# Kernel optimization log

Hardware: AMD Instinct MI355X
Metric: run time of the kernel (lower is better)

The kernel has to match this reference:

```python
import jax, jax.numpy as jnp
import numpy as np

E, D, H, T = 8, 1024, 2048, 2048  # num_expert, d_model, d_hidden, tokens

def setup_inputs() -> dict:
    key = jax.random.key(0)
    ks = jax.random.split(key, 7)
    return {
        "moe_inp": jax.random.normal(ks[0], (T, D), jnp.float32),
        "Wg": jax.random.normal(ks[1], (D, E), jnp.float32) * 0.02,
        "bg": jnp.zeros((E,), jnp.float32),
        "W1": jax.random.normal(ks[2], (E, D, H), jnp.float32) * 0.02,
        "b1": jnp.zeros((E, H), jnp.float32),
        "W2": jax.random.normal(ks[3], (E, H, D), jnp.float32) * 0.02,
        "b2": jnp.zeros((E, D), jnp.float32),
        "top_k": 2,
    }

def reference(moe_inp, Wg, bg, W1, b1, W2, b2, top_k):
    # NaiveGate: linear gate, top-k select, softmax over the selected logits
    logits = moe_inp @ Wg + bg                      # [T, E]
    top_vals, top_idx = jax.lax.top_k(logits, top_k)  # [T, k]
    gate_score = jax.nn.softmax(top_vals, axis=-1)    # [T, k]

    # Exact (no capacity drop) MoE: scan over experts, mask-combine.
    # Equivalent math to scatter -> per-expert FFN -> gather -> bmm(gate_score, ...).
    def body(acc, xs):
        e, w1, bb1, w2, bb2 = xs
        h = jax.nn.gelu(moe_inp @ w1 + bb1)          # [T, H]
        y = h @ w2 + bb2                             # [T, D]
        w = jnp.sum(jnp.where(top_idx == e, gate_score, 0.0), axis=-1)  # [T]
        return acc + w[:, None] * y, None

    init = jnp.zeros_like(moe_inp)
    xs = (jnp.arange(E), W1, b1, W2, b2)
    moe_outp, _ = jax.lax.scan(body, init, xs)
    return moe_outp, top_idx
```

## Files before the change

kernel.cpp:

```cpp
#include <hip/hip_runtime.h>
#include <stdint.h>

#define T_TOK 2048
#define D_DIM 1024
#define H_DIM 2048
#define N_EXP 8
#define MAXS  4608

#define WS_CNT    0
#define WS_BTOK   256
#define WS_BW     (WS_BTOK + N_EXP*2048*4)
#define WS_XG     (WS_BW + N_EXP*2048*4)
#define WS_HBUF   (WS_XG + (size_t)MAXS*1024*2)
#define WS_W1T    (WS_HBUF + (size_t)MAXS*2048*2)
#define WS_W2T    (WS_W1T + (size_t)N_EXP*1024*2048*2)

typedef __bf16 bf16x8 __attribute__((ext_vector_type(8)));
typedef float  f32x4  __attribute__((ext_vector_type(4)));

#define AS1 __attribute__((address_space(1)))
#define AS3 __attribute__((address_space(3)))

__device__ __forceinline__ unsigned short f2bf(float f) {
  unsigned int u = __float_as_uint(f);
  u += 0x7fffu + ((u >> 16) & 1u);
  return (unsigned short)(u >> 16);
}

__device__ __forceinline__ float gelu_tanh(float x) {
  const float u = 0.7978845608028654f * (x + 0.044715f * x * x * x);
  const float t = __expf(-2.0f * fabsf(u));
  const float th = (1.0f - t) * __builtin_amdgcn_rcpf(1.0f + t);
  return 0.5f * x * (1.0f + copysignf(th, u));
}


__device__ __forceinline__ void transpose_body(const float* __restrict__ in,
                                               unsigned short* __restrict__ out,
                                               int Rout, int Cin, int tx, int ty,
                                               void* smem_) {
  char* lds = (char*)smem_;
  const int c0 = tx * 64, r0 = ty * 64;
  const int tid = threadIdx.x;
  const int w = tid >> 6, l = tid & 63;
  const int lr = l >> 4;
  const int lc4 = (l & 15) * 4;
#pragma unroll
  for (int p = 0; p < 4; ++p) {
    const int rr = p * 16 + w * 4 + lr;
    const int c = lc4 ^ ((rr & 7) << 2);
    const float* src = in + (size_t)(r0 + rr) * Cin + (c0 + c);
    __builtin_amdgcn_global_load_lds((const AS1 void*)src,
                                     (AS3 void*)(lds + (size_t)rr * 256 + lc4 * 4),
                                     16, 0, 0);
  }
  __syncthreads();
  unsigned u[2][4];
#pragma unroll
  for (int p = 0; p < 2; ++p) {
    const int idx = p * 256 + tid;
    const int oc = idx >> 3, seg = idx & 7;
#pragma unroll
    for (int j = 0; j < 4; ++j) {
      const int ra = seg * 8 + 2 * j, rb = ra + 1;
      const float va = *(const float*)(lds + ra * 256 + ((oc ^ ((ra & 7) << 2)) * 4));
      const float vb = *(const float*)(lds + rb * 256 + ((oc ^ ((rb & 7) << 2)) * 4));
      u[p][j] = (unsigned)f2bf(va) | ((unsigned)f2bf(vb) << 16);
    }
  }
#pragma unroll
  for (int p = 0; p < 2; ++p) {
    const int idx = p * 256 + tid;
    const int oc = idx >> 3, seg = idx & 7;
    *(uint4*)(out + (size_t)(c0 + oc) * Rout + r0 + seg * 8) =
        make_uint4(u[p][0], u[p][1], u[p][2], u[p][3]);
  }
}

__device__ __forceinline__ void gate_body(int t, const float* __restrict__ x,
                                          const float* __restrict__ Wg,
                                          const float* __restrict__ bg,
                                          float* __restrict__ out_idx,
                                          int* __restrict__ cnt, int* __restrict__ btok,
                                          float* __restrict__ bw) {
  const int lane = threadIdx.x & 63;
  float p[8];
#pragma unroll
  for (int i = 0; i < 8; ++i) p[i] = 0.f;
  const float* xr = x + (size_t)t * D_DIM;
  for (int i = lane; i < D_DIM; i += 64) {
    const float xv = xr[i];
    const float4 wa = ((const float4*)(Wg + i * 8))[0];
    const float4 wb = ((const float4*)(Wg + i * 8))[1];
    p[0] += xv * wa.x; p[1] += xv * wa.y; p[2] += xv * wa.z; p[3] += xv * wa.w;
    p[4] += xv * wb.x; p[5] += xv * wb.y; p[6] += xv * wb.z; p[7] += xv * wb.w;
  }
#pragma unroll
  for (int off = 32; off > 0; off >>= 1) {
#pragma unroll
    for (int i = 0; i < 8; ++i) p[i] += __shfl_xor(p[i], off);
  }
  if (lane == 0) {
#pragma unroll
    for (int i = 0; i < 8; ++i) p[i] += bg[i];
    int i0 = 0; float v0 = p[0];
#pragma unroll
    for (int i = 1; i < 8; ++i) if (p[i] > v0) { v0 = p[i]; i0 = i; }
    int i1 = -1; float v1 = -3.4e38f;
#pragma unroll
    for (int i = 0; i < 8; ++i) if (i != i0 && p[i] > v1) { v1 = p[i]; i1 = i; }
    const float ex = expf(v1 - v0);
    const float inv = 1.f / (1.f + ex);
    out_idx[t * 2 + 0] = (float)i0;
    out_idx[t * 2 + 1] = (float)i1;
    int s0 = atomicAdd(&cnt[i0], 1);
    btok[i0 * 2048 + s0] = t; bw[i0 * 2048 + s0] = inv;
    int s1 = atomicAdd(&cnt[i1], 1);
    btok[i1 * 2048 + s1] = t; bw[i1 * 2048 + s1] = ex * inv;
  }
}

__device__ __forceinline__ void expert_seg(const int* __restrict__ cnt, int e,
                                           int& base, int& ce, int& pcnt, int& total) {
  int off = 0; base = 0; ce = 0; pcnt = 0;
#pragma unroll
  for (int i = 0; i < N_EXP; ++i) {
    const int c = cnt[i];
    const int p = (c + 63) & ~63;
    if (i == e) { base = off; ce = c; pcnt = p; }
    off += p;
  }
  total = off;
}

template <int MODE>
__device__ __forceinline__ void gemm_body(
    int lin, const float* __restrict__ X, const unsigned short* __restrict__ A,
    const unsigned short* __restrict__ B,
    const float* __restrict__ bias, const int* __restrict__ cnt,
    const int* __restrict__ btok, const float* __restrict__ bw,
    unsigned short* __restrict__ Hout, float* __restrict__ out, void* smem_) {
  constexpr int K   = (MODE == 0) ? D_DIM : H_DIM;
  constexpr int SK  = (MODE == 0) ? 1 : 2;
  constexpr int KS  = K / SK;
  constexpr int NIT = KS / 32;

  const int glo = lin & 7;
  const int mt  = (lin >> 3) & 31;
  const int g   = ((lin >> 8) << 3) | glo;
  int nt, e, ksl;
  if (MODE == 0) { nt = g & 15; e = g >> 4; ksl = 0; }
  else           { nt = g & 7;  e = (g >> 3) & 7; ksl = g >> 6; }

  int base, ce, pcnt, total;
  expert_seg(cnt, e, base, ce, pcnt, total);
  if (mt * 64 >= pcnt) return;
  const int row0 = base + mt * 64;
  const int n0 = nt * 128;

  unsigned short (*As)[64 * 32] = (unsigned short (*)[64 * 32])smem_;
  unsigned short (*Bs)[128 * 32] = (unsigned short (*)[128 * 32])((char*)smem_ + 8192);

  const int tid = threadIdx.x;
  const int lane = tid & 63;
  const int wv = tid >> 6;
  const int wm = wv >> 1;
  const int wn = wv & 1;

  const unsigned short* Bb = B + (size_t)e * ((size_t)H_DIM * D_DIM) + (size_t)n0 * K + ksl * KS;

  f32x4 acc[2][4];
#pragma unroll
  for (int i = 0; i < 2; ++i)
#pragma unroll
    for (int j = 0; j < 4; ++j) acc[i][j] = (f32x4)(0.0f);

  const int subr = lane >> 2;
  const int ksf = (lane & 3) * 8;
  const int fr = lane & 15;
  const int kq = (lane >> 4) * 8;

  const unsigned short* Ab = nullptr;
  const float* a_src = nullptr;
  bool a_real = false;
  if constexpr (MODE == 0) {
    const int al = mt * 64 + wv * 16 + subr;
    a_real = (al < ce);
    const int tok = a_real ? btok[e * 2048 + al] : 0;
    a_src = X + (size_t)tok * D_DIM + ksf;
  } else {
    Ab = A + (size_t)row0 * K + ksl * KS;
  }

  float4 pa0, pa1;
  auto stageA_load = [&](int kt) {
    if constexpr (MODE == 0) {
      if (a_real) {
        pa0 = *(const float4*)(a_src + kt * 32);
        pa1 = *(const float4*)(a_src + kt * 32 + 4);
      } else {
        pa0 = make_float4(0.f, 0.f, 0.f, 0.f);
        pa1 = make_float4(0.f, 0.f, 0.f, 0.f);
      }
    }
  };
  auto stageA_write = [&](int b) {
    if constexpr (MODE == 0) {
      uint4 u;
      u.x = (unsigned)f2bf(pa0.x) | ((unsigned)f2bf(pa0.y) << 16);
      u.y = (unsigned)f2bf(pa0.z) | ((unsigned)f2bf(pa0.w) << 16);
      u.z = (unsigned)f2bf(pa1.x) | ((unsigned)f2bf(pa1.y) << 16);
      u.w = (unsigned)f2bf(pa1.z) | ((unsigned)f2bf(pa1.w) << 16);
      *(uint4*)(As[b] + (wv * 16 + subr) * 32 + ksf) = u;
    }
  };
  auto stage = [&](int kt, int b) {
    const int k0 = kt * 32;
    if constexpr (MODE == 1) {
      const int r = wv * 16 + subr;
      const unsigned short* ga = Ab + (size_t)r * K + (k0 + ksf);
      __builtin_amdgcn_global_load_lds(
          (const AS1 void*)ga,
          (AS3 void*)(As[b] + wv * 16 * 32), 16, 0, 0);
    }
#pragma unroll
    for (int it = 0; it < 2; ++it) {
      const int ci = wv + it * 4;
      const int r = ci * 16 + subr;
      const unsigned short* gb = Bb + (size_t)r * K + (k0 + ksf);
      __builtin_amdgcn_global_load_lds(
          (const AS1 void*)gb,
          (AS3 void*)(Bs[b] + ci * 16 * 32), 16, 0, 0);
    }
  };

  stageA_load(0);
  stage(0, 0);
  stageA_write(0);
  for (int i = 0; i < NIT; ++i) {
    const int b = i & 1;
    __syncthreads();
    if (i + 1 < NIT) { stageA_load(i + 1); stage(i + 1, b ^ 1); }
    bf16x8 av[2], bv[4];
#pragma unroll
    for (int mi = 0; mi < 2; ++mi)
      av[mi] = *(const bf16x8*)(As[b] + (wm * 32 + mi * 16 + fr) * 32 + kq);
#pragma unroll
    for (int ni = 0; ni < 4; ++ni)
      bv[ni] = *(const bf16x8*)(Bs[b] + (wn * 64 + ni * 16 + fr) * 32 + kq);
#pragma unroll
    for (int mi = 0; mi < 2; ++mi)
#pragma unroll
      for (int ni = 0; ni < 4; ++ni)
        acc[mi][ni] = __builtin_amdgcn_mfma_f32_16x16x32_bf16(av[mi], bv[ni], acc[mi][ni], 0, 0, 0);
    if (i + 1 < NIT) stageA_write(b ^ 1);
  }

  if (MODE == 0) {
    const float* bb = bias + (size_t)e * H_DIM + n0;
#pragma unroll
    for (int mi = 0; mi < 2; ++mi) {
      const int rb = wm * 32 + mi * 16 + (lane >> 4) * 4;
#pragma unroll
      for (int r = 0; r < 4; ++r) {
        unsigned short* hp = Hout + (size_t)(row0 + rb + r) * H_DIM + n0;
#pragma unroll
        for (int ni = 0; ni < 4; ++ni) {
          const int col = wn * 64 + ni * 16 + fr;
          hp[col] = f2bf(gelu_tanh(acc[mi][ni][r] + bb[col]));
        }
      }
    }
  } else {
    const float* bb = bias + (size_t)e * D_DIM + n0;
#pragma unroll
    for (int mi = 0; mi < 2; ++mi) {
      const int rb = wm * 32 + mi * 16 + (lane >> 4) * 4;
#pragma unroll
      for (int r = 0; r < 4; ++r) {
        const int local = mt * 64 + rb + r;
        if (local < ce) {
          const int tok = btok[e * 2048 + local];
          const float w = bw[e * 2048 + local];
          float* op = out + (size_t)tok * D_DIM + n0;
#pragma unroll
          for (int ni = 0; ni < 4; ++ni) {
            const int col = wn * 64 + ni * 16 + fr;
            const float bias_once = (ksl == 0) ? bb[col] : 0.f;
            atomicAdd(op + col, w * (acc[mi][ni][r] + bias_once));
          }
        }
      }
    }
  }
}


__global__ void __launch_bounds__(256) prep_kernel(
    const float* __restrict__ x, const float* __restrict__ Wg,
    const float* __restrict__ bg, const float* __restrict__ W1,
    float* __restrict__ out, int* __restrict__ cnt, int* __restrict__ btok,
    float* __restrict__ bw, unsigned short* __restrict__ W1t) {
  __shared__ __align__(16) char smem[16384];
  const int bid = blockIdx.x;
  if (bid < 2048) {
    ((float4*)out)[bid * 256 + threadIdx.x] = make_float4(0.f, 0.f, 0.f, 0.f);
  } else if (bid < 2560) {
    gate_body((bid - 2048) * 4 + (threadIdx.x >> 6), x, Wg, bg,
              out + (size_t)T_TOK * D_DIM, cnt, btok, bw);
  } else {
    const int lin = bid - 2560;
    const int e = lin >> 9, l9 = lin & 511;
    transpose_body(W1 + (size_t)e * (D_DIM * H_DIM), W1t + (size_t)e * (D_DIM * H_DIM),
                   D_DIM, H_DIM, l9 & 31, l9 >> 5, smem);
  }
}

__global__ void __launch_bounds__(256) gemm0_w2t(
    const float* __restrict__ x, const unsigned short* __restrict__ W1t,
    const float* __restrict__ b1, const int* __restrict__ cnt,
    const int* __restrict__ btok, const float* __restrict__ bw,
    unsigned short* __restrict__ Hbuf, const float* __restrict__ W2,
    unsigned short* __restrict__ W2t) {
  __shared__ __align__(16) char smem[24576];
  if (blockIdx.x < 4096) {
    gemm_body<0>(blockIdx.x, x, nullptr, W1t, b1, cnt, btok, bw, Hbuf, nullptr, smem);
  } else {
    const int lin = blockIdx.x - 4096;
    const int e = lin >> 9, l9 = lin & 511;
    transpose_body(W2 + (size_t)e * (D_DIM * H_DIM), W2t + (size_t)e * (D_DIM * H_DIM),
                   H_DIM, D_DIM, l9 & 15, l9 >> 4, smem);
  }
}

__global__ void __launch_bounds__(256) moe_gemm1(
    const unsigned short* __restrict__ Hbuf, const unsigned short* __restrict__ W2t,
    const float* __restrict__ b2, const int* __restrict__ cnt,
    const int* __restrict__ btok, const float* __restrict__ bw,
    float* __restrict__ out) {
  __shared__ __align__(16) char smem[24576];
  gemm_body<1>(blockIdx.x, nullptr, Hbuf, W2t, b2, cnt, btok, bw, nullptr, out, smem);
}

extern "C" void kernel_launch(void* const* d_in, const int* in_sizes, int n_in,
                              void* d_out, int out_size, void* d_ws, size_t ws_size,
                              hipStream_t stream) {
  const float* moe_inp = (const float*)d_in[0];
  const float* Wg = (const float*)d_in[1];
  const float* bg = (const float*)d_in[2];
  const float* W1 = (const float*)d_in[3];
  const float* b1 = (const float*)d_in[4];
  const float* W2 = (const float*)d_in[5];
  const float* b2 = (const float*)d_in[6];
  float* out = (float*)d_out;

  char* ws = (char*)d_ws;
  int* cnt  = (int*)(ws + WS_CNT);
  int* btok = (int*)(ws + WS_BTOK);
  float* bw = (float*)(ws + WS_BW);
  unsigned short* Hbuf = (unsigned short*)(ws + WS_HBUF);
  unsigned short* W1t  = (unsigned short*)(ws + WS_W1T);
  unsigned short* W2t  = (unsigned short*)(ws + WS_W2T);

  hipMemsetAsync(cnt, 0, 256, stream);
  prep_kernel<<<dim3(6656), dim3(256), 0, stream>>>(moe_inp, Wg, bg, W1,
                                                    out, cnt, btok, bw, W1t);
  gemm0_w2t<<<dim3(8192), dim3(256), 0, stream>>>(moe_inp, W1t, b1, cnt, btok, bw,
                                                  Hbuf, W2, W2t);
  moe_gemm1<<<dim3(4096), dim3(256), 0, stream>>>(Hbuf, W2t, b2, cnt, btok, bw, out);
}
```

Measured before the change: 319.7 us.

## Merge three MoE kernels into one cooperative persistent kernel with grid syncs

Replaces the memset plus three kernel launches with a single cooperative persistent kernel. It walks the zero-init, gate/W1-transpose, GEMM0/W2-transpose and GEMM1 phases in grid-stride loops, with grid.sync between phases. The weight transpose also changes from direct global-to-LDS async loads with XOR swizzle to plain float4 loads into a padded LDS tile. The aim is to remove launch gaps and tail effects between stages, at the cost of grid-wide barriers, a grid sized by the occupancy query, and possibly slower transpose loads.

```diff
diff --git a/kernel.cpp b/kernel.cpp
--- a/kernel.cpp
+++ b/kernel.cpp
@@ -1,5 +1,8 @@
 #include <hip/hip_runtime.h>
+#include <hip/hip_cooperative_groups.h>
 #include <stdint.h>
+
+namespace cg = cooperative_groups;
 
 #define T_TOK 2048
 #define D_DIM 1024
@@ -39,41 +42,28 @@
                                                unsigned short* __restrict__ out,
                                                int Rout, int Cin, int tx, int ty,
                                                void* smem_) {
-  char* lds = (char*)smem_;
+  float (*tile)[68] = (float (*)[68])smem_;
   const int c0 = tx * 64, r0 = ty * 64;
   const int tid = threadIdx.x;
-  const int w = tid >> 6, l = tid & 63;
-  const int lr = l >> 4;
-  const int lc4 = (l & 15) * 4;
 #pragma unroll
   for (int p = 0; p < 4; ++p) {
-    const int rr = p * 16 + w * 4 + lr;
-    const int c = lc4 ^ ((rr & 7) << 2);
-    const float* src = in + (size_t)(r0 + rr) * Cin + (c0 + c);
-    __builtin_amdgcn_global_load_lds((const AS1 void*)src,
-                                     (AS3 void*)(lds + (size_t)rr * 256 + lc4 * 4),
-                                     16, 0, 0);
+    const int idx = p * 256 + tid;
+    const int r = idx >> 4, c4 = idx & 15;
+    *(float4*)&tile[r][c4 * 4] = *(const float4*)(in + (size_t)(r0 + r) * Cin + c0 + c4 * 4);
   }
   __syncthreads();
-  unsigned u[2][4];
 #pragma unroll
   for (int p = 0; p < 2; ++p) {
     const int idx = p * 256 + tid;
     const int oc = idx >> 3, seg = idx & 7;
+    unsigned u[4];
 #pragma unroll
     for (int j = 0; j < 4; ++j) {
-      const int ra = seg * 8 + 2 * j, rb = ra + 1;
-      const float va = *(const float*)(lds + ra * 256 + ((oc ^ ((ra & 7) << 2)) * 4));
-      const float vb = *(const float*)(lds + rb * 256 + ((oc ^ ((rb & 7) << 2)) * 4));
-      u[p][j] = (unsigned)f2bf(va) | ((unsigned)f2bf(vb) << 16);
-    }
-  }
-#pragma unroll
-  for (int p = 0; p < 2; ++p) {
-    const int idx = p * 256 + tid;
-    const int oc = idx >> 3, seg = idx & 7;
-    *(uint4*)(out + (size_t)(c0 + oc) * Rout + r0 + seg * 8) =
-        make_uint4(u[p][0], u[p][1], u[p][2], u[p][3]);
+      const unsigned lo = f2bf(tile[seg * 8 + 2 * j][oc]);
+      const unsigned hi = f2bf(tile[seg * 8 + 2 * j + 1][oc]);
+      u[j] = lo | (hi << 16);
+    }
+    *(uint4*)(out + (size_t)(c0 + oc) * Rout + r0 + seg * 8) = make_uint4(u[0], u[1], u[2], u[3]);
   }
 }
 
@@ -295,51 +285,59 @@
   }
 }
 
-
-__global__ void __launch_bounds__(256) prep_kernel(
+__global__ void __launch_bounds__(256, 4) moe_mega(
     const float* __restrict__ x, const float* __restrict__ Wg,
     const float* __restrict__ bg, const float* __restrict__ W1,
-    float* __restrict__ out, int* __restrict__ cnt, int* __restrict__ btok,
-    float* __restrict__ bw, unsigned short* __restrict__ W1t) {
-  __shared__ __align__(16) char smem[16384];
-  const int bid = blockIdx.x;
-  if (bid < 2048) {
-    ((float4*)out)[bid * 256 + threadIdx.x] = make_float4(0.f, 0.f, 0.f, 0.f);
-  } else if (bid < 2560) {
-    gate_body((bid - 2048) * 4 + (threadIdx.x >> 6), x, Wg, bg,
-              out + (size_t)T_TOK * D_DIM, cnt, btok, bw);
-  } else {
-    const int lin = bid - 2560;
-    const int e = lin >> 9, l9 = lin & 511;
-    transpose_body(W1 + (size_t)e * (D_DIM * H_DIM), W1t + (size_t)e * (D_DIM * H_DIM),
-                   D_DIM, H_DIM, l9 & 31, l9 >> 5, smem);
-  }
-}
-
-__global__ void __launch_bounds__(256) gemm0_w2t(
-    const float* __restrict__ x, const unsigned short* __restrict__ W1t,
-    const float* __restrict__ b1, const int* __restrict__ cnt,
-    const int* __restrict__ btok, const float* __restrict__ bw,
-    unsigned short* __restrict__ Hbuf, const float* __restrict__ W2,
+    const float* __restrict__ b1, const float* __restrict__ W2,
+    const float* __restrict__ b2, float* __restrict__ out,
+    int* __restrict__ cnt, int* __restrict__ btok, float* __restrict__ bw,
+    unsigned short* __restrict__ Hbuf, unsigned short* __restrict__ W1t,
     unsigned short* __restrict__ W2t) {
   __shared__ __align__(16) char smem[24576];
-  if (blockIdx.x < 4096) {
-    gemm_body<0>(blockIdx.x, x, nullptr, W1t, b1, cnt, btok, bw, Hbuf, nullptr, smem);
-  } else {
-    const int lin = blockIdx.x - 4096;
-    const int e = lin >> 9, l9 = lin & 511;
-    transpose_body(W2 + (size_t)e * (D_DIM * H_DIM), W2t + (size_t)e * (D_DIM * H_DIM),
-                   H_DIM, D_DIM, l9 & 15, l9 >> 4, smem);
-  }
-}
-
-__global__ void __launch_bounds__(256) moe_gemm1(
-    const unsigned short* __restrict__ Hbuf, const unsigned short* __restrict__ W2t,
-    const float* __restrict__ b2, const int* __restrict__ cnt,
-    const int* __restrict__ btok, const float* __restrict__ bw,
-    float* __restrict__ out) {
-  __shared__ __align__(16) char smem[24576];
-  gemm_body<1>(blockIdx.x, nullptr, Hbuf, W2t, b2, cnt, btok, bw, nullptr, out, smem);
+  cg::grid_group grid = cg::this_grid();
+  const int NB = gridDim.x;
+  const int bid = blockIdx.x;
+  const int tid = threadIdx.x;
+
+  for (int it = bid; it < 2048; it += NB)
+    ((float4*)out)[(size_t)it * 256 + tid] = make_float4(0.f, 0.f, 0.f, 0.f);
+  if (bid == 0 && tid < N_EXP) cnt[tid] = 0;
+  __threadfence();
+  grid.sync();
+
+  for (int it = bid; it < 4608; it += NB) {
+    if (it < 512) {
+      gate_body(it * 4 + (tid >> 6), x, Wg, bg, out + (size_t)T_TOK * D_DIM,
+                cnt, btok, bw);
+    } else {
+      const int lin = it - 512;
+      const int e = lin >> 9, l9 = lin & 511;
+      transpose_body(W1 + (size_t)e * (D_DIM * H_DIM), W1t + (size_t)e * (D_DIM * H_DIM),
+                     D_DIM, H_DIM, l9 & 31, l9 >> 5, smem);
+    }
+    __syncthreads();
+  }
+  __threadfence();
+  grid.sync();
+
+  for (int it = bid; it < 8192; it += NB) {
+    if (it < 4096) {
+      gemm_body<0>(it, x, nullptr, W1t, b1, cnt, btok, bw, Hbuf, nullptr, smem);
+    } else {
+      const int lin = it - 4096;
+      const int e = lin >> 9, l9 = lin & 511;
+      transpose_body(W2 + (size_t)e * (D_DIM * H_DIM), W2t + (size_t)e * (D_DIM * H_DIM),
+                     H_DIM, D_DIM, l9 & 15, l9 >> 4, smem);
+    }
+    __syncthreads();
+  }
+  __threadfence();
+  grid.sync();
+
+  for (int it = bid; it < 4096; it += NB) {
+    gemm_body<1>(it, nullptr, Hbuf, W2t, b2, cnt, btok, bw, nullptr, out, smem);
+    __syncthreads();
+  }
 }
 
 extern "C" void kernel_launch(void* const* d_in, const int* in_sizes, int n_in,
@@ -362,10 +360,14 @@
   unsigned short* W1t  = (unsigned short*)(ws + WS_W1T);
   unsigned short* W2t  = (unsigned short*)(ws + WS_W2T);
 
-  hipMemsetAsync(cnt, 0, 256, stream);
-  prep_kernel<<<dim3(6656), dim3(256), 0, stream>>>(moe_inp, Wg, bg, W1,
-                                                    out, cnt, btok, bw, W1t);
-  gemm0_w2t<<<dim3(8192), dim3(256), 0, stream>>>(moe_inp, W1t, b1, cnt, btok, bw,
-                                                  Hbuf, W2, W2t);
-  moe_gemm1<<<dim3(4096), dim3(256), 0, stream>>>(Hbuf, W2t, b2, cnt, btok, bw, out);
-}
+  int maxb = 0;
+  if (hipOccupancyMaxActiveBlocksPerMultiprocessor(&maxb, moe_mega, 256, 0) != hipSuccess
+      || maxb <= 0) maxb = 2;
+  if (maxb > 8) maxb = 8;
+  int nb = maxb * 256;
+
+  void* args[] = {(void*)&moe_inp, (void*)&Wg, (void*)&bg, (void*)&W1, (void*)&b1,
+                  (void*)&W2, (void*)&b2, (void*)&out, (void*)&cnt, (void*)&btok,
+                  (void*)&bw, (void*)&Hbuf, (void*)&W1t, (void*)&W2t};
+  hipLaunchCooperativeKernel(moe_mega, dim3(nb), dim3(256), args, 0, stream);
+}
```

Measured after the change: 928.2 us. 190% more time.

## Split prep into W1 transpose and gate kernels, use padded LDS transpose

Applied to the files above, without the earlier changes.

Replaces the async global_load_lds plus XOR-swizzled LDS transpose with plain float4 loads into a 68-float padded LDS tile. Splits the combined prep kernel into a dedicated W1 transpose kernel, which also zeroes the expert counters and so removes the memset, followed by a gate+output-zeroing kernel. This drops one memset launch and simplifies the transpose, at the cost of an extra kernel launch and the loss of direct-to-LDS loads. Padding of 4 floats may still leave some LDS bank conflicts in the column reads.

```diff
diff --git a/kernel.cpp b/kernel.cpp
--- a/kernel.cpp
+++ b/kernel.cpp
@@ -39,41 +39,28 @@
                                                unsigned short* __restrict__ out,
                                                int Rout, int Cin, int tx, int ty,
                                                void* smem_) {
-  char* lds = (char*)smem_;
+  float (*tile)[68] = (float (*)[68])smem_;
   const int c0 = tx * 64, r0 = ty * 64;
   const int tid = threadIdx.x;
-  const int w = tid >> 6, l = tid & 63;
-  const int lr = l >> 4;
-  const int lc4 = (l & 15) * 4;
 #pragma unroll
   for (int p = 0; p < 4; ++p) {
-    const int rr = p * 16 + w * 4 + lr;
-    const int c = lc4 ^ ((rr & 7) << 2);
-    const float* src = in + (size_t)(r0 + rr) * Cin + (c0 + c);
-    __builtin_amdgcn_global_load_lds((const AS1 void*)src,
-                                     (AS3 void*)(lds + (size_t)rr * 256 + lc4 * 4),
-                                     16, 0, 0);
+    const int idx = p * 256 + tid;
+    const int r = idx >> 4, c4 = idx & 15;
+    *(float4*)&tile[r][c4 * 4] = *(const float4*)(in + (size_t)(r0 + r) * Cin + c0 + c4 * 4);
   }
   __syncthreads();
-  unsigned u[2][4];
 #pragma unroll
   for (int p = 0; p < 2; ++p) {
     const int idx = p * 256 + tid;
     const int oc = idx >> 3, seg = idx & 7;
+    unsigned u[4];
 #pragma unroll
     for (int j = 0; j < 4; ++j) {
-      const int ra = seg * 8 + 2 * j, rb = ra + 1;
-      const float va = *(const float*)(lds + ra * 256 + ((oc ^ ((ra & 7) << 2)) * 4));
-      const float vb = *(const float*)(lds + rb * 256 + ((oc ^ ((rb & 7) << 2)) * 4));
-      u[p][j] = (unsigned)f2bf(va) | ((unsigned)f2bf(vb) << 16);
-    }
-  }
-#pragma unroll
-  for (int p = 0; p < 2; ++p) {
-    const int idx = p * 256 + tid;
-    const int oc = idx >> 3, seg = idx & 7;
-    *(uint4*)(out + (size_t)(c0 + oc) * Rout + r0 + seg * 8) =
-        make_uint4(u[p][0], u[p][1], u[p][2], u[p][3]);
+      const unsigned lo = f2bf(tile[seg * 8 + 2 * j][oc]);
+      const unsigned hi = f2bf(tile[seg * 8 + 2 * j + 1][oc]);
+      u[j] = lo | (hi << 16);
+    }
+    *(uint4*)(out + (size_t)(c0 + oc) * Rout + r0 + seg * 8) = make_uint4(u[0], u[1], u[2], u[3]);
   }
 }
 
@@ -296,23 +283,27 @@
 }
 
 
-__global__ void __launch_bounds__(256) prep_kernel(
+__global__ void __launch_bounds__(256) w1t_kernel(const float* __restrict__ W1,
+                                                  unsigned short* __restrict__ W1t,
+                                                  int* __restrict__ cnt) {
+  __shared__ __align__(16) char smem[17408];
+  if (blockIdx.x == 0 && blockIdx.y == 0 && threadIdx.x < N_EXP) cnt[threadIdx.x] = 0;
+  const int e = blockIdx.y;
+  const int lin = blockIdx.x;
+  transpose_body(W1 + (size_t)e * (D_DIM * H_DIM), W1t + (size_t)e * (D_DIM * H_DIM),
+                 D_DIM, H_DIM, lin & 31, lin >> 5, smem);
+}
+
+__global__ void __launch_bounds__(256) gate_zero_kernel(
     const float* __restrict__ x, const float* __restrict__ Wg,
-    const float* __restrict__ bg, const float* __restrict__ W1,
-    float* __restrict__ out, int* __restrict__ cnt, int* __restrict__ btok,
-    float* __restrict__ bw, unsigned short* __restrict__ W1t) {
-  __shared__ __align__(16) char smem[16384];
+    const float* __restrict__ bg, float* __restrict__ out,
+    int* __restrict__ cnt, int* __restrict__ btok, float* __restrict__ bw) {
   const int bid = blockIdx.x;
   if (bid < 2048) {
     ((float4*)out)[bid * 256 + threadIdx.x] = make_float4(0.f, 0.f, 0.f, 0.f);
-  } else if (bid < 2560) {
+  } else {
     gate_body((bid - 2048) * 4 + (threadIdx.x >> 6), x, Wg, bg,
               out + (size_t)T_TOK * D_DIM, cnt, btok, bw);
-  } else {
-    const int lin = bid - 2560;
-    const int e = lin >> 9, l9 = lin & 511;
-    transpose_body(W1 + (size_t)e * (D_DIM * H_DIM), W1t + (size_t)e * (D_DIM * H_DIM),
-                   D_DIM, H_DIM, l9 & 31, l9 >> 5, smem);
   }
 }
 
@@ -362,9 +353,9 @@
   unsigned short* W1t  = (unsigned short*)(ws + WS_W1T);
   unsigned short* W2t  = (unsigned short*)(ws + WS_W2T);
 
-  hipMemsetAsync(cnt, 0, 256, stream);
-  prep_kernel<<<dim3(6656), dim3(256), 0, stream>>>(moe_inp, Wg, bg, W1,
-                                                    out, cnt, btok, bw, W1t);
+  w1t_kernel<<<dim3(512, N_EXP), dim3(256), 0, stream>>>(W1, W1t, cnt);
+  gate_zero_kernel<<<dim3(2560), dim3(256), 0, stream>>>(moe_inp, Wg, bg, out,
+                                                         cnt, btok, bw);
   gemm0_w2t<<<dim3(8192), dim3(256), 0, stream>>>(moe_inp, W1t, b1, cnt, btok, bw,
                                                   Hbuf, W2, W2t);
   moe_gemm1<<<dim3(4096), dim3(256), 0, stream>>>(Hbuf, W2t, b2, cnt, btok, bw, out);
```

Result: slower. 329.3 us (+3.0%).
